# Performance work log

Hardware: AMD Instinct MI355X
Metric: run time of the kernel (lower is better)

## Reference

```python
import jax, jax.numpy as jnp
import numpy as np

N_LEVELS = 12
N_FEATURES = 2
HASH_SIZE = 1 << 14  # 16384
BASE_RESOLUTION = 16
PER_LEVEL_SCALE = 2.0
BATCH = 4_194_304


def _resolutions():
    # matches the torch loop: int(round(cur)) with cur *= per_level_scale
    res = []
    cur = float(BASE_RESOLUTION)
    for _ in range(N_LEVELS):
        res.append(int(round(cur)))
        cur *= PER_LEVEL_SCALE
    return jnp.asarray(res, dtype=jnp.float32)  # [L]


def setup_inputs() -> dict:
    key = jax.random.key(0)
    k1, k2 = jax.random.split(key)
    x = jax.random.uniform(k1, (BATCH,), dtype=jnp.float32)
    # learned hash table, init uniform(-1e-4, 1e-4) like the torch module
    table = jax.random.uniform(
        k2, (HASH_SIZE, N_LEVELS * N_FEATURES), dtype=jnp.float32,
        minval=-1e-4, maxval=1e-4,
    )
    return {"x": x, "table": table}


def reference(x, table):
    # x: [B] in [0,1]; table: [HASH_SIZE, L*F]
    res = _resolutions()                       # [L]
    xc = jnp.clip(x, 0.0, 1.0)                 # [B]
    pos = xc[:, None] * res[None, :]           # [B, L] -- all levels at once
    i0 = jnp.floor(pos).astype(jnp.int32)      # [B, L]
    w = (pos - i0.astype(pos.dtype))[..., None]  # [B, L, 1]
    h0 = i0 % HASH_SIZE                        # [B, L]
    h1 = (i0 + 1) % HASH_SIZE                  # [B, L]
    emb3 = table.reshape(HASH_SIZE, N_LEVELS, N_FEATURES)  # [H, L, F]
    lvl = jnp.arange(N_LEVELS)[None, :]        # [1, L]
    e0 = emb3[h0, lvl]                         # [B, L, F] gather per level
    e1 = emb3[h1, lvl]                         # [B, L, F]
    feats = (1.0 - w) * e0 + w * e1            # [B, L, F]
    # torch concatenates per-level [B,F] slices -> level-major layout
    return feats.reshape(x.shape[0], N_LEVELS * N_FEATURES)
```

## Files before the change

### kernel.cpp

```cpp
#include <hip/hip_runtime.h>

#define HASH_SIZE 16384
#define N_LEVELS 12

__global__ __launch_bounds__(256) void HashGrid1D_kernel(
    const float* __restrict__ x,
    const float* __restrict__ table,
    float* __restrict__ out,
    int total)
{
    int idx = blockIdx.x * blockDim.x + threadIdx.x;
    if (idx >= total) return;

    int b = idx / N_LEVELS;
    int l = idx - b * N_LEVELS;

    float xv = x[b];
    float xc = fminf(fmaxf(xv, 0.0f), 1.0f);

    float res = (float)(16 << l);

    float pos = xc * res;
    float fi  = floorf(pos);
    int   i0  = (int)fi;
    float w   = pos - fi;

    int h0 = i0 & (HASH_SIZE - 1);
    int h1 = (i0 + 1) & (HASH_SIZE - 1);

    int off0 = h0 * (N_LEVELS * 2) + l * 2;
    int off1 = h1 * (N_LEVELS * 2) + l * 2;
    const float2 e0 = *reinterpret_cast<const float2*>(table + off0);
    const float2 e1 = *reinterpret_cast<const float2*>(table + off1);

    float omw = 1.0f - w;
    float2 r;
    r.x = omw * e0.x + w * e1.x;
    r.y = omw * e0.y + w * e1.y;

    *reinterpret_cast<float2*>(out + (size_t)idx * 2) = r;
}

extern "C" void kernel_launch(void* const* d_in, const int* in_sizes, int n_in,
                              void* d_out, int out_size, void* d_ws, size_t ws_size,
                              hipStream_t stream) {
    const float* x     = (const float*)d_in[0];
    const float* table = (const float*)d_in[1];
    float* out         = (float*)d_out;

    int batch = in_sizes[0];
    int total = batch * N_LEVELS;

    int block = 256;
    int grid  = (total + block - 1) / block;

    HashGrid1D_kernel<<<grid, block, 0, stream>>>(x, table, out, total);
}
```

Measured before the change: 585.2 us.

## Prebuild level-major paired-corner table and process two levels per thread

A pre-pass kernel rewrites the hash table into a level-major workspace where each entry holds both interpolation corners as one float4. The main kernel then does a single 16-byte gather per level, handles two levels per thread, and writes float4 outputs. The aim is fewer gather instructions, better locality per level, and wider stores. The cost is an extra launch and a 3 MB workspace, and if the workspace is too small the code falls back to the direct kernel.

```diff
diff --git a/kernel.cpp b/kernel.cpp
--- a/kernel.cpp
+++ b/kernel.cpp
@@ -1,9 +1,60 @@
 #include <hip/hip_runtime.h>
 
 #define HASH_SIZE 16384
-#define N_LEVELS 12
+#define N_LEVELS  12
+#define LP        6
 
-__global__ __launch_bounds__(256) void HashGrid1D_kernel(
+__global__ __launch_bounds__(256) void build_ws_kernel(
+    const float* __restrict__ table,
+    float4* __restrict__ ws4)
+{
+    int tid = blockIdx.x * blockDim.x + threadIdx.x;
+    if (tid >= N_LEVELS * HASH_SIZE) return;
+    int l  = tid >> 14;
+    int h  = tid & (HASH_SIZE - 1);
+    int h1 = (h + 1) & (HASH_SIZE - 1);
+    const float2 e0 = *reinterpret_cast<const float2*>(table + h  * (N_LEVELS * 2) + l * 2);
+    const float2 e1 = *reinterpret_cast<const float2*>(table + h1 * (N_LEVELS * 2) + l * 2);
+    ws4[tid] = make_float4(e0.x, e0.y, e1.x, e1.y);
+}
+
+__global__ __launch_bounds__(256) void hashgrid_main_kernel(
+    const float* __restrict__ x,
+    const float4* __restrict__ ws4,
+    float4* __restrict__ out4,
+    int total)
+{
+    int t = blockIdx.x * blockDim.x + threadIdx.x;
+    if (t >= total) return;
+
+    int b = t / LP;
+    int p = t - b * LP;
+
+    float xc = fminf(fmaxf(x[b], 0.0f), 1.0f);
+
+    float4 r;
+    #pragma unroll
+    for (int k = 0; k < 2; ++k) {
+        int   lvl = p * 2 + k;
+        float res = (float)(16 << lvl);
+        float pos = xc * res;
+        float fi  = floorf(pos);
+        float w   = pos - fi;
+        int   h0  = ((int)fi) & (HASH_SIZE - 1);
+
+        float4 e = ws4[lvl * HASH_SIZE + h0];
+
+        float omw = 1.0f - w;
+        float r0 = omw * e.x + w * e.z;
+        float r1 = omw * e.y + w * e.w;
+        if (k == 0) { r.x = r0; r.y = r1; }
+        else        { r.z = r0; r.w = r1; }
+    }
+
+    out4[t] = r;
+}
+
+__global__ __launch_bounds__(256) void hashgrid_direct_kernel(
     const float* __restrict__ x,
     const float* __restrict__ table,
     float* __restrict__ out,
@@ -11,34 +62,23 @@
 {
     int idx = blockIdx.x * blockDim.x + threadIdx.x;
     if (idx >= total) return;
-
     int b = idx / N_LEVELS;
     int l = idx - b * N_LEVELS;
-
-    float xv = x[b];
-    float xc = fminf(fmaxf(xv, 0.0f), 1.0f);
-
+    float xc  = fminf(fmaxf(x[b], 0.0f), 1.0f);
     float res = (float)(16 << l);
-
     float pos = xc * res;
     float fi  = floorf(pos);
     int   i0  = (int)fi;
     float w   = pos - fi;
-
     int h0 = i0 & (HASH_SIZE - 1);
     int h1 = (i0 + 1) & (HASH_SIZE - 1);
-
-    int off0 = h0 * (N_LEVELS * 2) + l * 2;
-    int off1 = h1 * (N_LEVELS * 2) + l * 2;
-    const float2 e0 = *reinterpret_cast<const float2*>(table + off0);
-    const float2 e1 = *reinterpret_cast<const float2*>(table + off1);
-
+    const float2 e0 = *reinterpret_cast<const float2*>(table + h0 * (N_LEVELS * 2) + l * 2);
+    const float2 e1 = *reinterpret_cast<const float2*>(table + h1 * (N_LEVELS * 2) + l * 2);
     float omw = 1.0f - w;
-    float2 r;
-    r.x = omw * e0.x + w * e1.x;
-    r.y = omw * e0.y + w * e1.y;
-
-    *reinterpret_cast<float2*>(out + (size_t)idx * 2) = r;
+    float2 rr;
+    rr.x = omw * e0.x + w * e1.x;
+    rr.y = omw * e0.y + w * e1.y;
+    *reinterpret_cast<float2*>(out + (size_t)idx * 2) = rr;
 }
 
 extern "C" void kernel_launch(void* const* d_in, const int* in_sizes, int n_in,
@@ -46,13 +86,22 @@
                               hipStream_t stream) {
     const float* x     = (const float*)d_in[0];
     const float* table = (const float*)d_in[1];
-    float* out         = (float*)d_out;
+    int batch = in_sizes[0];
 
-    int batch = in_sizes[0];
-    int total = batch * N_LEVELS;
+    const size_t ws_needed = (size_t)N_LEVELS * HASH_SIZE * sizeof(float4);
 
-    int block = 256;
-    int grid  = (total + block - 1) / block;
+    if (ws_size >= ws_needed) {
+        float4* ws4 = (float4*)d_ws;
 
-    HashGrid1D_kernel<<<grid, block, 0, stream>>>(x, table, out, total);
+        int ta = N_LEVELS * HASH_SIZE;
+        build_ws_kernel<<<(ta + 255) / 256, 256, 0, stream>>>(table, ws4);
+
+        int total = batch * LP;
+        hashgrid_main_kernel<<<(total + 255) / 256, 256, 0, stream>>>(
+            x, ws4, (float4*)d_out, total);
+    } else {
+        int total = batch * N_LEVELS;
+        hashgrid_direct_kernel<<<(total + 255) / 256, 256, 0, stream>>>(
+            x, table, (float*)d_out, total);
+    }
 }
```

Result: faster. 506.7 us (-13.4%).
